# Kernel tuning notes

Hardware: AMD Instinct MI355X
Metric: run time of the kernel (lower is better)

The kernel has to match this reference:

```python
import jax, jax.numpy as jnp
import numpy as np

NOISE_LEVEL = 0.05  # midpoint of uniform(0.01, 0.1) in the original
A_COEF = 0.99
B_COEF = 0.01


def setup_inputs() -> dict:
    key = jax.random.key(0)
    k1, k2 = jax.random.split(key)
    C, T = 256, 220500
    waveform = jax.random.normal(k1, (C, T), dtype=jnp.float32)
    white_noise = jax.random.normal(k2, (C, T), dtype=jnp.float32)
    return {"waveform": waveform, "white_noise": white_noise}


def _pink_noise(white_noise):
    # First-order IIR: f[0] = w[0]; f[i] = 0.99*f[i-1] + 0.01*w[i]
    # Vectorized over channels, lax.scan over time.
    w0 = white_noise[:, 0]                      # [C]
    wt = white_noise[:, 1:].T                   # [T-1, C]

    def step(carry, w_t):
        f = A_COEF * carry + B_COEF * w_t
        return f, f

    _, rest = jax.lax.scan(step, w0, wt)        # rest: [T-1, C]
    pink = jnp.concatenate([w0[None, :], rest], axis=0).T  # [C, T]
    return pink


def reference(waveform, white_noise):
    pink = _pink_noise(white_noise)
    mixed = waveform + pink * NOISE_LEVEL
    max_val = jnp.max(jnp.abs(mixed))
    # normalize only if peak exceeds 1.0
    return jnp.where(max_val > 1.0, mixed / max_val, mixed)
```

## Files before the change

kernel.cpp:

```cpp
#include <hip/hip_runtime.h>


#define TLEN 220500
#define CHANNELS 256

constexpr int CL   = 8192;
constexpr int H    = 1024;
constexpr int NT   = 256;
constexpr int SEG  = 32;
constexpr int WSEG = 4;
constexpr int NCHUNK = (TLEN + CL - 1) / CL;

constexpr float AC = 0.99f;
constexpr float BC = 0.01f;
constexpr float NL = 0.05f;

constexpr double dpow(double a, int n) { double r = 1.0; for (int i = 0; i < n; ++i) r *= a; return r; }
constexpr float A_SEG  = (float)dpow(0.99, SEG);
constexpr float A_WSEG = (float)dpow(0.99, WSEG);

__device__ __forceinline__ int maddr(int j) { return (j >> 5) * 33 + (j & 31); }
__device__ __forceinline__ int waddr(int j) { return (j >> 2) * 5 + (j & 3); }

__global__ void init_max_kernel(unsigned int* gmax) { *gmax = 0u; }

__global__ __launch_bounds__(NT, 4)
void pink_mix_kernel(const float* __restrict__ waveform,
                     const float* __restrict__ white,
                     float* __restrict__ out,
                     unsigned int* __restrict__ gmax)
{
    __shared__ float lm[NT * 33];
    __shared__ float lw[NT * 5];
    __shared__ float sA[4], sB[4], swA[4], swB[4], sM[4];

    const int chunk = blockIdx.x;
    const int ch    = blockIdx.y;
    const int c0    = chunk * CL;
    const size_t rowoff = (size_t)ch * TLEN;
    const float* __restrict__ wrow = white + rowoff;
    const float* __restrict__ arow = waveform + rowoff;
    float* __restrict__ orow = out + rowoff;

    const int tid  = threadIdx.x;
    const int lane = tid & 63;
    const int wv   = tid >> 6;

    #pragma unroll
    for (int i = 0; i < SEG / 4; ++i) {
        int j4 = i * NT + tid;
        int g  = c0 + 4 * j4;
        float4 v = make_float4(0.f, 0.f, 0.f, 0.f);
        if (g < TLEN) v = *reinterpret_cast<const float4*>(wrow + g);
        int base = maddr(4 * j4);
        lm[base] = v.x; lm[base + 1] = v.y; lm[base + 2] = v.z; lm[base + 3] = v.w;
    }
    if (chunk > 0) {
        int g = c0 - H + 4 * tid;
        float4 v = *reinterpret_cast<const float4*>(wrow + g);
        int base = waddr(4 * tid);
        lw[base] = v.x; lw[base + 1] = v.y; lw[base + 2] = v.z; lw[base + 3] = v.w;
    }
    __syncthreads();

    const float w0first = lm[0];

    if (chunk > 0) {
        float f = 0.f;
        #pragma unroll
        for (int k = 0; k < WSEG; ++k)
            f = fmaf(AC, f, BC * lw[tid * 5 + k]);
        float pA = A_WSEG, pB = f;
        #pragma unroll
        for (int d = 1; d < 64; d <<= 1) {
            float oA = __shfl_up(pA, d, 64);
            float oB = __shfl_up(pB, d, 64);
            if (lane >= d) { pB = fmaf(pA, oB, pB); pA *= oA; }
        }
        if (lane == 63) { swA[wv] = pA; swB[wv] = pB; }
    }

    float f = 0.f;
    #pragma unroll
    for (int k = 0; k < SEG; ++k)
        f = fmaf(AC, f, BC * lm[tid * 33 + k]);
    float pA = A_SEG, pB = f;
    #pragma unroll
    for (int d = 1; d < 64; d <<= 1) {
        float oA = __shfl_up(pA, d, 64);
        float oB = __shfl_up(pB, d, 64);
        if (lane >= d) { pB = fmaf(pA, oB, pB); pA *= oA; }
    }
    float eA = __shfl_up(pA, 1, 64);
    float eB = __shfl_up(pB, 1, 64);
    if (lane == 0) { eA = 1.f; eB = 0.f; }
    if (lane == 63) { sA[wv] = pA; sB[wv] = pB; }
    __syncthreads();

    float fin;
    if (chunk > 0) {
        float tA = swA[0], tB = swB[0];
        #pragma unroll
        for (int w = 1; w < 4; ++w) { tB = fmaf(swA[w], tB, swB[w]); tA *= swA[w]; }
        fin = tB;
    } else {
        fin = w0first;
    }

    float wA = 1.f, wB = 0.f;
    for (int w = 0; w < wv; ++w) { wB = fmaf(sA[w], wB, sB[w]); wA *= sA[w]; }
    float tA = eA * wA;
    float tB = fmaf(eA, wB, eB);
    float fe = fmaf(tA, fin, tB);

    f = fe;
    #pragma unroll
    for (int k = 0; k < SEG; ++k) {
        int a = tid * 33 + k;
        float w = lm[a];
        f = fmaf(AC, f, BC * w);
        lm[a] = f;
    }
    __syncthreads();

    float mx = 0.f;
    #pragma unroll
    for (int i = 0; i < SEG / 4; ++i) {
        int j4 = i * NT + tid;
        int g  = c0 + 4 * j4;
        if (g < TLEN) {
            int base = maddr(4 * j4);
            float4 wf = *reinterpret_cast<const float4*>(arow + g);
            float4 m;
            m.x = fmaf(NL, lm[base],     wf.x);
            m.y = fmaf(NL, lm[base + 1], wf.y);
            m.z = fmaf(NL, lm[base + 2], wf.z);
            m.w = fmaf(NL, lm[base + 3], wf.w);
            *reinterpret_cast<float4*>(orow + g) = m;
            mx = fmaxf(mx, fmaxf(fmaxf(fabsf(m.x), fabsf(m.y)),
                                 fmaxf(fabsf(m.z), fabsf(m.w))));
        }
    }
    #pragma unroll
    for (int d = 32; d >= 1; d >>= 1)
        mx = fmaxf(mx, __shfl_xor(mx, d, 64));
    if (lane == 0) sM[wv] = mx;
    __syncthreads();
    if (tid == 0) {
        float m = fmaxf(fmaxf(sM[0], sM[1]), fmaxf(sM[2], sM[3]));
        atomicMax(gmax, __float_as_uint(m));
    }
}

__global__ __launch_bounds__(256)
void scale_kernel(float* __restrict__ out, const unsigned int* __restrict__ gmax, int n4)
{
    const float m = __uint_as_float(*gmax);
    const float s = (m > 1.0f) ? (1.0f / m) : 1.0f;
    float4* p = reinterpret_cast<float4*>(out);
    int i = blockIdx.x * blockDim.x + threadIdx.x;
    const int stride = gridDim.x * blockDim.x;
    for (; i < n4; i += stride) {
        float4 v = p[i];
        v.x *= s; v.y *= s; v.z *= s; v.w *= s;
        p[i] = v;
    }
}

extern "C" void kernel_launch(void* const* d_in, const int* in_sizes, int n_in,
                              void* d_out, int out_size, void* d_ws, size_t ws_size,
                              hipStream_t stream)
{
    const float* waveform = (const float*)d_in[0];
    const float* white    = (const float*)d_in[1];
    float* out            = (float*)d_out;
    unsigned int* gmax    = (unsigned int*)d_ws;

    hipLaunchKernelGGL(init_max_kernel, dim3(1), dim3(1), 0, stream, gmax);

    dim3 grid(NCHUNK, CHANNELS);
    hipLaunchKernelGGL(pink_mix_kernel, grid, dim3(NT), 0, stream,
                       waveform, white, out, gmax);

    const int n4 = out_size / 4;
    hipLaunchKernelGGL(scale_kernel, dim3(2048), dim3(256), 0, stream,
                       out, gmax, n4);
}
```

Measured before the change: 242.2 us.

## Keep per-thread segments in registers and use constant decay powers in scan

Each thread now loads its contiguous 32-sample segment straight into registers with strided float4 loads, replacing the padded LDS staging and its extra barrier. The scan drops the multiplicative A component because decay powers are compile-time constants, and the per-thread prefix factor is computed with exp2. It also raises the launch-bounds occupancy hint and enlarges the scale kernel grid. The trade-off is that global loads are no longer coalesced across threads (each thread reads its own 128-byte span), and register pressure rises.

```diff
diff --git a/kernel.cpp b/kernel.cpp
--- a/kernel.cpp
+++ b/kernel.cpp
@@ -8,7 +8,6 @@
 constexpr int H    = 1024;
 constexpr int NT   = 256;
 constexpr int SEG  = 32;
-constexpr int WSEG = 4;
 constexpr int NCHUNK = (TLEN + CL - 1) / CL;
 
 constexpr float AC = 0.99f;
@@ -16,23 +15,34 @@
 constexpr float NL = 0.05f;
 
 constexpr double dpow(double a, int n) { double r = 1.0; for (int i = 0; i < n; ++i) r *= a; return r; }
-constexpr float A_SEG  = (float)dpow(0.99, SEG);
-constexpr float A_WSEG = (float)dpow(0.99, WSEG);
 
-__device__ __forceinline__ int maddr(int j) { return (j >> 5) * 33 + (j & 31); }
-__device__ __forceinline__ int waddr(int j) { return (j >> 2) * 5 + (j & 3); }
+constexpr float SP0 = (float)dpow(0.99, 32 * 1);
+constexpr float SP1 = (float)dpow(0.99, 32 * 2);
+constexpr float SP2 = (float)dpow(0.99, 32 * 4);
+constexpr float SP3 = (float)dpow(0.99, 32 * 8);
+constexpr float SP4 = (float)dpow(0.99, 32 * 16);
+constexpr float SP5 = (float)dpow(0.99, 32 * 32);
+constexpr float WP0 = (float)dpow(0.99, 4 * 1);
+constexpr float WP1 = (float)dpow(0.99, 4 * 2);
+constexpr float WP2 = (float)dpow(0.99, 4 * 4);
+constexpr float WP3 = (float)dpow(0.99, 4 * 8);
+constexpr float WP4 = (float)dpow(0.99, 4 * 16);
+constexpr float WP5 = (float)dpow(0.99, 4 * 32);
+constexpr float AWW = (float)dpow(0.99, 256);
+constexpr float L2ASEG = -0.4639862302435683f;
 
 __global__ void init_max_kernel(unsigned int* gmax) { *gmax = 0u; }
 
-__global__ __launch_bounds__(NT, 4)
+__global__ __launch_bounds__(NT, 6)
 void pink_mix_kernel(const float* __restrict__ waveform,
                      const float* __restrict__ white,
                      float* __restrict__ out,
                      unsigned int* __restrict__ gmax)
 {
-    __shared__ float lm[NT * 33];
-    __shared__ float lw[NT * 5];
-    __shared__ float sA[4], sB[4], swA[4], swB[4], sM[4];
+    __shared__ float sB[4];
+    __shared__ float swB[4];
+    __shared__ float sM[4];
+    __shared__ float sW0;
 
     const int chunk = blockIdx.x;
     const int ch    = blockIdx.y;
@@ -45,102 +55,90 @@
     const int tid  = threadIdx.x;
     const int lane = tid & 63;
     const int wv   = tid >> 6;
+    const int s0   = c0 + tid * SEG;
 
+    float w[SEG];
     #pragma unroll
     for (int i = 0; i < SEG / 4; ++i) {
-        int j4 = i * NT + tid;
-        int g  = c0 + 4 * j4;
+        int g = s0 + 4 * i;
         float4 v = make_float4(0.f, 0.f, 0.f, 0.f);
         if (g < TLEN) v = *reinterpret_cast<const float4*>(wrow + g);
-        int base = maddr(4 * j4);
-        lm[base] = v.x; lm[base + 1] = v.y; lm[base + 2] = v.z; lm[base + 3] = v.w;
+        w[4 * i]     = v.x;
+        w[4 * i + 1] = v.y;
+        w[4 * i + 2] = v.z;
+        w[4 * i + 3] = v.w;
     }
-    if (chunk > 0) {
-        int g = c0 - H + 4 * tid;
-        float4 v = *reinterpret_cast<const float4*>(wrow + g);
-        int base = waddr(4 * tid);
-        lw[base] = v.x; lw[base + 1] = v.y; lw[base + 2] = v.z; lw[base + 3] = v.w;
-    }
-    __syncthreads();
-
-    const float w0first = lm[0];
 
     if (chunk > 0) {
+        float4 v = *reinterpret_cast<const float4*>(wrow + (c0 - H) + 4 * tid);
         float f = 0.f;
-        #pragma unroll
-        for (int k = 0; k < WSEG; ++k)
-            f = fmaf(AC, f, BC * lw[tid * 5 + k]);
-        float pA = A_WSEG, pB = f;
-        #pragma unroll
-        for (int d = 1; d < 64; d <<= 1) {
-            float oA = __shfl_up(pA, d, 64);
-            float oB = __shfl_up(pB, d, 64);
-            if (lane >= d) { pB = fmaf(pA, oB, pB); pA *= oA; }
-        }
-        if (lane == 63) { swA[wv] = pA; swB[wv] = pB; }
+        f = fmaf(AC, f, BC * v.x);
+        f = fmaf(AC, f, BC * v.y);
+        f = fmaf(AC, f, BC * v.z);
+        f = fmaf(AC, f, BC * v.w);
+        float pB = f;
+        { float o = __shfl_up(pB, 1,  64); if (lane >= 1)  pB = fmaf(WP0, o, pB); }
+        { float o = __shfl_up(pB, 2,  64); if (lane >= 2)  pB = fmaf(WP1, o, pB); }
+        { float o = __shfl_up(pB, 4,  64); if (lane >= 4)  pB = fmaf(WP2, o, pB); }
+        { float o = __shfl_up(pB, 8,  64); if (lane >= 8)  pB = fmaf(WP3, o, pB); }
+        { float o = __shfl_up(pB, 16, 64); if (lane >= 16) pB = fmaf(WP4, o, pB); }
+        { float o = __shfl_up(pB, 32, 64); if (lane >= 32) pB = fmaf(WP5, o, pB); }
+        if (lane == 63) swB[wv] = pB;
     }
 
     float f = 0.f;
     #pragma unroll
     for (int k = 0; k < SEG; ++k)
-        f = fmaf(AC, f, BC * lm[tid * 33 + k]);
-    float pA = A_SEG, pB = f;
-    #pragma unroll
-    for (int d = 1; d < 64; d <<= 1) {
-        float oA = __shfl_up(pA, d, 64);
-        float oB = __shfl_up(pB, d, 64);
-        if (lane >= d) { pB = fmaf(pA, oB, pB); pA *= oA; }
-    }
-    float eA = __shfl_up(pA, 1, 64);
+        f = fmaf(AC, f, BC * w[k]);
+    float pB = f;
+    { float o = __shfl_up(pB, 1,  64); if (lane >= 1)  pB = fmaf(SP0, o, pB); }
+    { float o = __shfl_up(pB, 2,  64); if (lane >= 2)  pB = fmaf(SP1, o, pB); }
+    { float o = __shfl_up(pB, 4,  64); if (lane >= 4)  pB = fmaf(SP2, o, pB); }
+    { float o = __shfl_up(pB, 8,  64); if (lane >= 8)  pB = fmaf(SP3, o, pB); }
+    { float o = __shfl_up(pB, 16, 64); if (lane >= 16) pB = fmaf(SP4, o, pB); }
+    { float o = __shfl_up(pB, 32, 64); if (lane >= 32) pB = fmaf(SP5, o, pB); }
     float eB = __shfl_up(pB, 1, 64);
-    if (lane == 0) { eA = 1.f; eB = 0.f; }
-    if (lane == 63) { sA[wv] = pA; sB[wv] = pB; }
+    if (lane == 0) eB = 0.f;
+    if (lane == 63) sB[wv] = pB;
+    if (tid == 0) sW0 = w[0];
     __syncthreads();
 
     float fin;
     if (chunk > 0) {
-        float tA = swA[0], tB = swB[0];
-        #pragma unroll
-        for (int w = 1; w < 4; ++w) { tB = fmaf(swA[w], tB, swB[w]); tA *= swA[w]; }
-        fin = tB;
+        float t = swB[0];
+        t = fmaf(AWW, t, swB[1]);
+        t = fmaf(AWW, t, swB[2]);
+        t = fmaf(AWW, t, swB[3]);
+        fin = t;
     } else {
-        fin = w0first;
+        fin = sW0;
     }
 
-    float wA = 1.f, wB = 0.f;
-    for (int w = 0; w < wv; ++w) { wB = fmaf(sA[w], wB, sB[w]); wA *= sA[w]; }
-    float tA = eA * wA;
-    float tB = fmaf(eA, wB, eB);
-    float fe = fmaf(tA, fin, tB);
+    constexpr float AW = (float)dpow(0.99, 2048);
+    float wB = 0.f;
+    for (int u = 0; u < wv; ++u) wB = fmaf(AW, wB, sB[u]);
+
+    const float fe = fmaf(__builtin_exp2f((float)tid  * L2ASEG), fin,
+                     fmaf(__builtin_exp2f((float)lane * L2ASEG), wB, eB));
 
     f = fe;
-    #pragma unroll
-    for (int k = 0; k < SEG; ++k) {
-        int a = tid * 33 + k;
-        float w = lm[a];
-        f = fmaf(AC, f, BC * w);
-        lm[a] = f;
-    }
-    __syncthreads();
-
     float mx = 0.f;
     #pragma unroll
     for (int i = 0; i < SEG / 4; ++i) {
-        int j4 = i * NT + tid;
-        int g  = c0 + 4 * j4;
+        int g = s0 + 4 * i;
         if (g < TLEN) {
-            int base = maddr(4 * j4);
-            float4 wf = *reinterpret_cast<const float4*>(arow + g);
+            float4 a = *reinterpret_cast<const float4*>(arow + g);
             float4 m;
-            m.x = fmaf(NL, lm[base],     wf.x);
-            m.y = fmaf(NL, lm[base + 1], wf.y);
-            m.z = fmaf(NL, lm[base + 2], wf.z);
-            m.w = fmaf(NL, lm[base + 3], wf.w);
+            f = fmaf(AC, f, BC * w[4 * i]);     m.x = fmaf(NL, f, a.x);
+            f = fmaf(AC, f, BC * w[4 * i + 1]); m.y = fmaf(NL, f, a.y);
+            f = fmaf(AC, f, BC * w[4 * i + 2]); m.z = fmaf(NL, f, a.z);
+            f = fmaf(AC, f, BC * w[4 * i + 3]); m.w = fmaf(NL, f, a.w);
             *reinterpret_cast<float4*>(orow + g) = m;
             mx = fmaxf(mx, fmaxf(fmaxf(fabsf(m.x), fabsf(m.y)),
                                  fmaxf(fabsf(m.z), fabsf(m.w))));
         }
     }
+
     #pragma unroll
     for (int d = 32; d >= 1; d >>= 1)
         mx = fmaxf(mx, __shfl_xor(mx, d, 64));
@@ -183,6 +181,6 @@
                        waveform, white, out, gmax);
 
     const int n4 = out_size / 4;
-    hipLaunchKernelGGL(scale_kernel, dim3(2048), dim3(256), 0, stream,
+    hipLaunchKernelGGL(scale_kernel, dim3(3072), dim3(256), 0, stream,
                        out, gmax, n4);
 }
```

After: 692.5 us. 186% more time.
